# Performance work log

Measured on AMD Instinct MI355X. Metric: run time of the kernel, lower is better.

## Reference

```python
import jax, jax.numpy as jnp
import numpy as np


def setup_inputs() -> dict:
    key = jax.random.key(0)
    ks = jax.random.split(key, 4)
    d, d_k, d_v = 1024, 128, 128
    B, S = 4, 4096
    scale = 1.0 / np.sqrt(d)
    return {
        "X": jax.random.normal(ks[0], (B, S, d), dtype=jnp.float32),
        "W_q": jax.random.normal(ks[1], (d, d_k), dtype=jnp.float32) * scale,
        "b_q": jnp.zeros((d_k,), dtype=jnp.float32),
        "W_k": jax.random.normal(ks[2], (d, d_k), dtype=jnp.float32) * scale,
        "b_k": jnp.zeros((d_k,), dtype=jnp.float32),
        "W_v": jax.random.normal(ks[3], (d, d_v), dtype=jnp.float32) * scale,
        "b_v": jnp.zeros((d_v,), dtype=jnp.float32),
    }


def reference(X, W_q, b_q, W_k, b_k, W_v, b_v):
    # Projections: [B, S, d_k/d_v]
    Q = jnp.einsum("bsd,dk->bsk", X, W_q) + b_q
    K = jnp.einsum("bsd,dk->bsk", X, W_k) + b_k
    V = jnp.einsum("bsd,dv->bsv", X, W_v) + b_v

    d_k = Q.shape[-1]
    # Scaled dot-product scores: [B, S, S]
    scores = jnp.einsum("bqk,bsk->bqs", Q, K) / jnp.sqrt(jnp.float32(d_k))
    # Causal (lower-triangular) mask
    S = scores.shape[-1]
    causal = jnp.tril(jnp.ones((S, S), dtype=bool))
    scores = jnp.where(causal[None, :, :], scores, -jnp.inf)
    weights = jax.nn.softmax(scores, axis=-1)
    # Weighted sum of values: [B, S, d_v]
    return jnp.einsum("bqs,bsv->bqv", weights, V)
```

## Files before the change

### kernel.cpp

```cpp
#include <hip/hip_runtime.h>
#include <hip/hip_bf16.h>
#include <stdint.h>


typedef __bf16 bf16x8 __attribute__((ext_vector_type(8)));
typedef float  f32x4  __attribute__((ext_vector_type(4)));
typedef unsigned int u32x4 __attribute__((ext_vector_type(4)));
typedef unsigned int u32x2 __attribute__((ext_vector_type(2)));

using bf16 = __hip_bfloat16;

#define AS1 __attribute__((address_space(1)))
#define AS3 __attribute__((address_space(3)))

__device__ __forceinline__ void gl_lds16(const void* g, void* l) {
  __builtin_amdgcn_global_load_lds((AS1 uint32_t*)g, (AS3 uint32_t*)l, 16, 0, 0);
}

__device__ __forceinline__ void wait_vm4() {
  asm volatile("s_waitcnt vmcnt(4)" ::: "memory");
  __builtin_amdgcn_sched_barrier(0);
}
__device__ __forceinline__ void wait_vm0() {
  asm volatile("s_waitcnt vmcnt(0)" ::: "memory");
  __builtin_amdgcn_sched_barrier(0);
}

__global__ __launch_bounds__(256) void k_wt(const float* __restrict__ Wq,
                                            const float* __restrict__ Wk,
                                            const float* __restrict__ Wv,
                                            bf16* __restrict__ Wt) {
  __shared__ bf16 t[64][72];
  const float* W = blockIdx.z == 0 ? Wq : (blockIdx.z == 1 ? Wk : Wv);
  int k0 = blockIdx.x * 64, n0 = blockIdx.y * 64;
  int tid = threadIdx.x;
  int r = tid >> 4, c4 = (tid & 15) * 4;
#pragma unroll
  for (int s = 0; s < 4; ++s) {
    int rr = r + s * 16;
    float4 v = *(const float4*)(W + (size_t)(k0 + rr) * 128 + n0 + c4);
    t[rr][c4 + 0] = __float2bfloat16(v.x);
    t[rr][c4 + 1] = __float2bfloat16(v.y);
    t[rr][c4 + 2] = __float2bfloat16(v.z);
    t[rr][c4 + 3] = __float2bfloat16(v.w);
  }
  __syncthreads();
  bf16* out = Wt + (size_t)blockIdx.z * 128 * 1024;
#pragma unroll
  for (int s = 0; s < 4; ++s) {
    int rn = r + s * 16;
    union { bf16 h[4]; u32x2 v; } u;
    u.h[0] = t[c4 + 0][rn]; u.h[1] = t[c4 + 1][rn];
    u.h[2] = t[c4 + 2][rn]; u.h[3] = t[c4 + 3][rn];
    *(u32x2*)(out + (size_t)(n0 + rn) * 1024 + k0 + c4) = u.v;
  }
}

__global__ __launch_bounds__(512) void k_qkv(const float* __restrict__ X,
                                             const bf16* __restrict__ Wt,
                                             const float* __restrict__ bq,
                                             const float* __restrict__ bk,
                                             const float* __restrict__ bv,
                                             bf16* __restrict__ Qo,
                                             bf16* __restrict__ Ko,
                                             bf16* __restrict__ Vt) {
  __shared__ __align__(16) char smem[65536];
  float* Xs = (float*)smem;
  bf16* Ws = (bf16*)(smem + 16384);
  bf16* Vs = (bf16*)smem;

  const int m0 = blockIdx.x * 64;
  const int tid = threadIdx.x;
  const int lane = tid & 63;
  const int li = lane & 15, g = lane >> 4;
  const int wid = tid >> 6;
  const int wm = wid >> 2, wn = wid & 3;

  const int xr = tid >> 3;
  const int xc32 = (tid & 7) >> 1;
  const int xhf = tid & 1;
  const int wr = tid >> 2;
  const int wc = tid & 3;

  f32x4 acc[3][2][2] = {};

  {
    gl_lds16(X + (size_t)(m0 + xr) * 1024 + (xc32 ^ (xr & 3)) * 8 + xhf * 4,
             Xs + tid * 4);
#pragma unroll
    for (int z = 0; z < 3; ++z)
      gl_lds16(Wt + (size_t)z * 131072 + (size_t)wr * 1024 + (wc ^ (wr & 3)) * 8,
               Ws + z * 4096 + tid * 8);
  }
  int cur = 0;
  for (int kt = 0; kt < 32; ++kt) {
    if (kt < 31) {
      const int k0 = (kt + 1) * 32;
      gl_lds16(X + (size_t)(m0 + xr) * 1024 + k0 + (xc32 ^ (xr & 3)) * 8 + xhf * 4,
               Xs + (cur ^ 1) * 2048 + tid * 4);
#pragma unroll
      for (int z = 0; z < 3; ++z)
        gl_lds16(Wt + (size_t)z * 131072 + (size_t)wr * 1024 + k0 + (wc ^ (wr & 3)) * 8,
                 Ws + (cur ^ 1) * 12288 + z * 4096 + tid * 8);
      wait_vm4();
    } else {
      wait_vm0();
    }
    __builtin_amdgcn_s_barrier();

    bf16x8 af[2];
#pragma unroll
    for (int mf = 0; mf < 2; ++mf) {
      int r = wm * 32 + mf * 16 + li;
      const float* xp = Xs + cur * 2048 + r * 32 + ((g ^ (r & 3)) * 8);
      f32x4 x0 = *(const f32x4*)xp;
      f32x4 x1 = *(const f32x4*)(xp + 4);
      union { bf16 h[8]; bf16x8 v; } u;
      u.h[0] = __float2bfloat16(x0[0]); u.h[1] = __float2bfloat16(x0[1]);
      u.h[2] = __float2bfloat16(x0[2]); u.h[3] = __float2bfloat16(x0[3]);
      u.h[4] = __float2bfloat16(x1[0]); u.h[5] = __float2bfloat16(x1[1]);
      u.h[6] = __float2bfloat16(x1[2]); u.h[7] = __float2bfloat16(x1[3]);
      af[mf] = u.v;
    }
#pragma unroll
    for (int z = 0; z < 3; ++z) {
#pragma unroll
      for (int nf = 0; nf < 2; ++nf) {
        int r = wn * 32 + nf * 16 + li;
        bf16x8 bfrag =
            *(const bf16x8*)(Ws + cur * 12288 + z * 4096 + r * 32 + ((g ^ (r & 3)) * 8));
#pragma unroll
        for (int mf = 0; mf < 2; ++mf)
          acc[z][mf][nf] = __builtin_amdgcn_mfma_f32_16x16x32_bf16(
              af[mf], bfrag, acc[z][mf][nf], 0, 0, 0);
      }
    }
    __builtin_amdgcn_s_barrier();
    cur ^= 1;
  }

#pragma unroll
  for (int z = 0; z < 2; ++z) {
    const float* bias = z == 0 ? bq : bk;
    bf16* Out = z == 0 ? Qo : Ko;
    const float scale = z == 0 ? 0.12752404368678202f : 1.0f;
#pragma unroll
    for (int nf = 0; nf < 2; ++nf) {
      int col = wn * 32 + nf * 16 + li;
      float bb = bias[col];
#pragma unroll
      for (int mf = 0; mf < 2; ++mf)
#pragma unroll
        for (int j = 0; j < 4; ++j) {
          int row = m0 + wm * 32 + mf * 16 + g * 4 + j;
          Out[(size_t)row * 128 + col] =
              __float2bfloat16((acc[z][mf][nf][j] + bb) * scale);
        }
    }
  }

  __syncthreads();
#pragma unroll
  for (int nf = 0; nf < 2; ++nf) {
    int col = wn * 32 + nf * 16 + li;
    float bb = bv[col];
#pragma unroll
    for (int mf = 0; mf < 2; ++mf)
#pragma unroll
      for (int j = 0; j < 4; ++j) {
        int row = wm * 32 + mf * 16 + g * 4 + j;
        Vs[row * 136 + col] = __float2bfloat16(acc[2][mf][nf][j] + bb);
      }
  }
  __syncthreads();
  const int b = m0 >> 12;
  const int s_off = m0 & 4095;
#pragma unroll
  for (int t2 = 0; t2 < 2; ++t2) {
    int idx = tid + 512 * t2;
    int dv = idx & 127;
    int sg = idx >> 7;
    union { bf16 h[8]; u32x4 v; } u;
#pragma unroll
    for (int si = 0; si < 8; ++si) u.h[si] = Vs[(sg * 8 + si) * 136 + dv];
    *(u32x4*)(Vt + (size_t)(b * 128 + dv) * 4096 + s_off + sg * 8) = u.v;
  }
}

__global__ __launch_bounds__(512, 4) void k_attn(const bf16* __restrict__ Qb,
                                                 const bf16* __restrict__ Kb,
                                                 const bf16* __restrict__ Vt,
                                                 bf16* __restrict__ o_part,
                                                 float* __restrict__ l_part) {
  __shared__ __align__(16) bf16 Kls[2][64 * 128];
  __shared__ __align__(16) bf16 Vls[2][128 * 64];
  __shared__ __align__(16) bf16 Pls[8][16 * 36];

  const int bid = blockIdx.x;
  const int xcd = bid & 7;
  const int slot = xcd * 72 + (bid >> 3);
  const int b = slot / 144;
  const int s = 143 - (slot - b * 144);
  const int widx = b * 144 + s;
  int qt = 0;
#pragma unroll
  for (int q2 = 1; q2 < 32; ++q2) {
    int M = q2 >> 2;
    if ((M + 1) * (2 * M + (q2 & 3)) <= s) qt = q2;
  }
  const int Mq = qt >> 2;
  const int chunk = s - (Mq + 1) * (2 * Mq + (qt & 3));
  const int ntiles = 2 * qt + 2;
  const int nch = (qt + 4) >> 2;
  const int clen = ntiles / nch;
  const int crem = ntiles - clen * nch;
  const int kt0 = chunk * clen + min(chunk, crem);
  const int kt1 = kt0 + clen + (chunk < crem ? 1 : 0) - 1;

  const int tid = threadIdx.x;
  const int lane = tid & 63;
  const int li = lane & 15, g = lane >> 4;
  const int w8 = tid >> 6;

  bf16x8 qf[4];
#pragma unroll
  for (int ks = 0; ks < 4; ++ks)
    qf[ks] = *(const bf16x8*)(Qb +
        (size_t)(b * 4096 + qt * 128 + w8 * 16 + li) * 128 + ks * 32 + g * 8);

  f32x4 o[8] = {};
  f32x4 lacc = {};
  bf16x8 ones;
#pragma unroll
  for (int e = 0; e < 8; ++e) ones[e] = (__bf16)1.0f;

  bf16* P = &Pls[w8][0];
  const bf16* Vtb = Vt + (size_t)b * 128 * 4096;

  {
    const int kv0 = kt0 * 64;
#pragma unroll
    for (int ii = 0; ii < 2; ++ii) {
      int c = tid + 512 * ii;
      int r = c >> 4, cc = c & 15;
      gl_lds16(Kb + (size_t)(b * 4096 + kv0 + r) * 128 + (cc ^ (r & 7)) * 8,
               &Kls[0][c * 8]);
      int r2 = c >> 3, cc2 = c & 7;
      gl_lds16(Vtb + (size_t)r2 * 4096 + kv0 + (cc2 ^ (r2 & 7)) * 8,
               &Vls[0][c * 8]);
    }
  }
  int cur = 0;
  for (int kt = kt0; kt <= kt1; ++kt) {
    if (kt < kt1) {
      const int kv0n = (kt + 1) * 64;
#pragma unroll
      for (int ii = 0; ii < 2; ++ii) {
        int c = tid + 512 * ii;
        int r = c >> 4, cc = c & 15;
        gl_lds16(Kb + (size_t)(b * 4096 + kv0n + r) * 128 + (cc ^ (r & 7)) * 8,
                 &Kls[cur ^ 1][c * 8]);
        int r2 = c >> 3, cc2 = c & 7;
        gl_lds16(Vtb + (size_t)r2 * 4096 + kv0n + (cc2 ^ (r2 & 7)) * 8,
                 &Vls[cur ^ 1][c * 8]);
      }
      wait_vm4();
    } else {
      wait_vm0();
    }
    __builtin_amdgcn_s_barrier();

    const bf16* Kl = &Kls[cur][0];
    const bf16* Vl = &Vls[cur][0];
    const int kv0 = kt * 64;

    f32x4 st[4] = {};
#pragma unroll
    for (int ks = 0; ks < 4; ++ks) {
      bf16x8 kf[4];
#pragma unroll
      for (int nf = 0; nf < 4; ++nf) {
        int r = nf * 16 + li;
        int ch = (ks * 4 + g) ^ (r & 7);
        kf[nf] = *(const bf16x8*)(Kl + r * 128 + ch * 8);
      }
#pragma unroll
      for (int nf = 0; nf < 4; ++nf)
        st[nf] = __builtin_amdgcn_mfma_f32_16x16x32_bf16(
            kf[nf], qf[ks], st[nf], 0, 0, 0);
    }

    if (kt >= 2 * qt) {
      const int dk = kv0 - qt * 128;
      const int qloc = w8 * 16 + li;
#pragma unroll
      for (int nf = 0; nf < 4; ++nf)
#pragma unroll
        for (int j = 0; j < 4; ++j)
          if (dk + nf * 16 + g * 4 + j > qloc) st[nf][j] = -1e30f;
    }

#pragma unroll
    for (int h = 0; h < 2; ++h) {
#pragma unroll
      for (int nfh = 0; nfh < 2; ++nfh) {
        const f32x4 sv = st[h * 2 + nfh];
        union { bf16 h4[4]; u32x2 v; } u;
#pragma unroll
        for (int j = 0; j < 4; ++j)
          u.h4[j] = __float2bfloat16(exp2f(sv[j]));
        *(u32x2*)(P + li * 36 + nfh * 16 + g * 4) = u.v;
      }
      bf16x8 pa = *(const bf16x8*)(P + li * 36 + g * 8);
#pragma unroll
      for (int dvf = 0; dvf < 8; ++dvf) {
        int r = dvf * 16 + li;
        int ch = (h * 4 + g) ^ (li & 7);
        bf16x8 vf = *(const bf16x8*)(Vl + r * 64 + ch * 8);
        o[dvf] = __builtin_amdgcn_mfma_f32_16x16x32_bf16(
            vf, pa, o[dvf], 0, 0, 0);
      }
      lacc = __builtin_amdgcn_mfma_f32_16x16x32_bf16(ones, pa, lacc, 0, 0, 0);
    }
    __builtin_amdgcn_s_barrier();
    cur ^= 1;
  }

  bf16* op = o_part + (size_t)widx * (128 * 128);
  float* lp = l_part + widx * 128;
  {
    const int qloc = w8 * 16 + li;
    if (g == 0) lp[qloc] = lacc[0];
#pragma unroll
    for (int dvf = 0; dvf < 8; ++dvf) {
      union { bf16 h4[4]; u32x2 v; } u;
#pragma unroll
      for (int j = 0; j < 4; ++j) u.h4[j] = __float2bfloat16(o[dvf][j]);
      *(u32x2*)(op + (size_t)qloc * 128 + dvf * 16 + g * 4) = u.v;
    }
  }
}

__global__ __launch_bounds__(256) void k_comb(const bf16* __restrict__ op,
                                              const float* __restrict__ lp,
                                              float* __restrict__ out) {
  int i = blockIdx.x * 256 + threadIdx.x;
  int row = i >> 4;
  int col8 = (i & 15) * 8;
  int b = row >> 12;
  int rb = row & 4095;
  int qt = rb >> 7;
  int lr = rb & 127;
  int M = qt >> 2;
  int base = b * 144 + (M + 1) * (2 * M + (qt & 3));
  int n = (qt + 4) >> 2;
  float l = 0.0f;
  float acc[8] = {};
  for (int c = 0; c < n; ++c) {
    l += lp[(base + c) * 128 + lr];
    union { bf16 h[8]; u32x4 v; } u;
    u.v = *(const u32x4*)(op + (size_t)(base + c) * 16384 + lr * 128 + col8);
#pragma unroll
    for (int j = 0; j < 8; ++j) acc[j] += __bfloat162float(u.h[j]);
  }
  float linv = 1.0f / l;
  float4 r0, r1;
  r0.x = acc[0] * linv; r0.y = acc[1] * linv;
  r0.z = acc[2] * linv; r0.w = acc[3] * linv;
  r1.x = acc[4] * linv; r1.y = acc[5] * linv;
  r1.z = acc[6] * linv; r1.w = acc[7] * linv;
  ((float4*)out)[i * 2] = r0;
  ((float4*)out)[i * 2 + 1] = r1;
}

extern "C" void kernel_launch(void* const* d_in, const int* in_sizes, int n_in,
                              void* d_out, int out_size, void* d_ws, size_t ws_size,
                              hipStream_t stream) {
  const float* X  = (const float*)d_in[0];
  const float* Wq = (const float*)d_in[1];
  const float* bq = (const float*)d_in[2];
  const float* Wk = (const float*)d_in[3];
  const float* bk = (const float*)d_in[4];
  const float* Wv = (const float*)d_in[5];
  const float* bv = (const float*)d_in[6];
  float* out = (float*)d_out;

  char* ws = (char*)d_ws;
  bf16* Wt  = (bf16*)(ws + 0);
  bf16* Qb  = (bf16*)(ws + 786432);
  bf16* Kb  = (bf16*)(ws + 4980736);
  bf16* Vt  = (bf16*)(ws + 9175040);
  bf16* o_part = (bf16*)(ws + 13369344);
  float* l_part = (float*)(ws + 32243712);

  k_wt<<<dim3(16, 2, 3), dim3(256), 0, stream>>>(Wq, Wk, Wv, Wt);
  k_qkv<<<dim3(256), dim3(512), 0, stream>>>(X, Wt, bq, bk, bv, Qb, Kb, Vt);
  k_attn<<<dim3(576), dim3(512), 0, stream>>>(Qb, Kb, Vt, o_part, l_part);
  k_comb<<<dim3(1024), dim3(256), 0, stream>>>(o_part, l_part, out);
}
```

Measured before the change: 85.05 us.

## Use 32x32x16 MFMA in attention with register-permuted P instead of LDS

The attention kernel now uses 4 waves of 32 query rows each (256 threads) instead of 8 waves of 16, and switches to 32x32x16 bf16 MFMAs for both QK^T and PV. The P matrix is now rearranged into the B-operand layout with ds_bpermute lane exchanges instead of a round trip through a per-wave LDS buffer. The aim is to raise MFMA efficiency, reduce K/V LDS reads per FLOP, and remove the LDS writes and reads of P. In exchange, accumulator register pressure per wave goes up, and there are fewer waves per block to hide load latency.

```diff
diff --git a/kernel.cpp b/kernel.cpp
--- a/kernel.cpp
+++ b/kernel.cpp
@@ -5,6 +5,7 @@
 
 typedef __bf16 bf16x8 __attribute__((ext_vector_type(8)));
 typedef float  f32x4  __attribute__((ext_vector_type(4)));
+typedef float  f32x16 __attribute__((ext_vector_type(16)));
 typedef unsigned int u32x4 __attribute__((ext_vector_type(4)));
 typedef unsigned int u32x2 __attribute__((ext_vector_type(2)));
 
@@ -19,6 +20,10 @@
 
 __device__ __forceinline__ void wait_vm4() {
   asm volatile("s_waitcnt vmcnt(4)" ::: "memory");
+  __builtin_amdgcn_sched_barrier(0);
+}
+__device__ __forceinline__ void wait_vm8() {
+  asm volatile("s_waitcnt vmcnt(8)" ::: "memory");
   __builtin_amdgcn_sched_barrier(0);
 }
 __device__ __forceinline__ void wait_vm0() {
@@ -187,14 +192,13 @@
   }
 }
 
-__global__ __launch_bounds__(512, 4) void k_attn(const bf16* __restrict__ Qb,
+__global__ __launch_bounds__(256, 2) void k_attn(const bf16* __restrict__ Qb,
                                                  const bf16* __restrict__ Kb,
                                                  const bf16* __restrict__ Vt,
                                                  bf16* __restrict__ o_part,
                                                  float* __restrict__ l_part) {
   __shared__ __align__(16) bf16 Kls[2][64 * 128];
   __shared__ __align__(16) bf16 Vls[2][128 * 64];
-  __shared__ __align__(16) bf16 Pls[8][16 * 36];
 
   const int bid = blockIdx.x;
   const int xcd = bid & 7;
@@ -219,29 +223,30 @@
 
   const int tid = threadIdx.x;
   const int lane = tid & 63;
-  const int li = lane & 15, g = lane >> 4;
-  const int w8 = tid >> 6;
-
-  bf16x8 qf[4];
-#pragma unroll
-  for (int ks = 0; ks < 4; ++ks)
-    qf[ks] = *(const bf16x8*)(Qb +
-        (size_t)(b * 4096 + qt * 128 + w8 * 16 + li) * 128 + ks * 32 + g * 8);
-
-  f32x4 o[8] = {};
-  f32x4 lacc = {};
+  const int l31 = lane & 31;
+  const int hl = lane >> 5;
+  const int w = tid >> 6;
+
+  const int qrow = b * 4096 + qt * 128 + w * 32 + l31;
+  bf16x8 qf[8];
+#pragma unroll
+  for (int ks = 0; ks < 8; ++ks)
+    qf[ks] = *(const bf16x8*)(Qb + (size_t)qrow * 128 + ks * 16 + hl * 8);
+
+  f32x16 o[4] = {};
+  f32x16 lacc = {};
   bf16x8 ones;
 #pragma unroll
   for (int e = 0; e < 8; ++e) ones[e] = (__bf16)1.0f;
 
-  bf16* P = &Pls[w8][0];
   const bf16* Vtb = Vt + (size_t)b * 128 * 4096;
+  const int xaddr = (lane ^ 32) << 2;
 
   {
     const int kv0 = kt0 * 64;
 #pragma unroll
-    for (int ii = 0; ii < 2; ++ii) {
-      int c = tid + 512 * ii;
+    for (int ii = 0; ii < 4; ++ii) {
+      int c = tid + 256 * ii;
       int r = c >> 4, cc = c & 15;
       gl_lds16(Kb + (size_t)(b * 4096 + kv0 + r) * 128 + (cc ^ (r & 7)) * 8,
                &Kls[0][c * 8]);
@@ -255,8 +260,8 @@
     if (kt < kt1) {
       const int kv0n = (kt + 1) * 64;
 #pragma unroll
-      for (int ii = 0; ii < 2; ++ii) {
-        int c = tid + 512 * ii;
+      for (int ii = 0; ii < 4; ++ii) {
+        int c = tid + 256 * ii;
         int r = c >> 4, cc = c & 15;
         gl_lds16(Kb + (size_t)(b * 4096 + kv0n + r) * 128 + (cc ^ (r & 7)) * 8,
                  &Kls[cur ^ 1][c * 8]);
@@ -264,7 +269,7 @@
         gl_lds16(Vtb + (size_t)r2 * 4096 + kv0n + (cc2 ^ (r2 & 7)) * 8,
                  &Vls[cur ^ 1][c * 8]);
       }
-      wait_vm4();
+      wait_vm8();
     } else {
       wait_vm0();
     }
@@ -274,53 +279,73 @@
     const bf16* Vl = &Vls[cur][0];
     const int kv0 = kt * 64;
 
-    f32x4 st[4] = {};
-#pragma unroll
-    for (int ks = 0; ks < 4; ++ks) {
-      bf16x8 kf[4];
-#pragma unroll
-      for (int nf = 0; nf < 4; ++nf) {
-        int r = nf * 16 + li;
-        int ch = (ks * 4 + g) ^ (r & 7);
-        kf[nf] = *(const bf16x8*)(Kl + r * 128 + ch * 8);
-      }
-#pragma unroll
-      for (int nf = 0; nf < 4; ++nf)
-        st[nf] = __builtin_amdgcn_mfma_f32_16x16x32_bf16(
-            kf[nf], qf[ks], st[nf], 0, 0, 0);
+    f32x16 st[2] = {};
+#pragma unroll
+    for (int ks = 0; ks < 8; ++ks) {
+#pragma unroll
+      for (int t = 0; t < 2; ++t) {
+        int r = t * 32 + l31;
+        int ch = (2 * ks + hl) ^ (r & 7);
+        bf16x8 kf = *(const bf16x8*)(Kl + r * 128 + ch * 8);
+        st[t] = __builtin_amdgcn_mfma_f32_32x32x16_bf16(
+            kf, qf[ks], st[t], 0, 0, 0);
+      }
     }
 
     if (kt >= 2 * qt) {
       const int dk = kv0 - qt * 128;
-      const int qloc = w8 * 16 + li;
-#pragma unroll
-      for (int nf = 0; nf < 4; ++nf)
-#pragma unroll
-        for (int j = 0; j < 4; ++j)
-          if (dk + nf * 16 + g * 4 + j > qloc) st[nf][j] = -1e30f;
-    }
-
-#pragma unroll
-    for (int h = 0; h < 2; ++h) {
-#pragma unroll
-      for (int nfh = 0; nfh < 2; ++nfh) {
-        const f32x4 sv = st[h * 2 + nfh];
-        union { bf16 h4[4]; u32x2 v; } u;
-#pragma unroll
-        for (int j = 0; j < 4; ++j)
-          u.h4[j] = __float2bfloat16(exp2f(sv[j]));
-        *(u32x2*)(P + li * 36 + nfh * 16 + g * 4) = u.v;
-      }
-      bf16x8 pa = *(const bf16x8*)(P + li * 36 + g * 8);
-#pragma unroll
-      for (int dvf = 0; dvf < 8; ++dvf) {
-        int r = dvf * 16 + li;
-        int ch = (h * 4 + g) ^ (li & 7);
-        bf16x8 vf = *(const bf16x8*)(Vl + r * 64 + ch * 8);
-        o[dvf] = __builtin_amdgcn_mfma_f32_16x16x32_bf16(
-            vf, pa, o[dvf], 0, 0, 0);
-      }
-      lacc = __builtin_amdgcn_mfma_f32_16x16x32_bf16(ones, pa, lacc, 0, 0, 0);
+      const int qloc = w * 32 + l31;
+#pragma unroll
+      for (int t = 0; t < 2; ++t)
+#pragma unroll
+        for (int reg = 0; reg < 16; ++reg) {
+          int kvl = dk + t * 32 + (reg & 3) + 8 * (reg >> 2) + 4 * hl;
+          if (kvl > qloc) st[t][reg] = -1e30f;
+        }
+    }
+
+    uint32_t D[2][8];
+#pragma unroll
+    for (int t = 0; t < 2; ++t)
+#pragma unroll
+      for (int i = 0; i < 8; ++i) {
+        union { bf16 h2[2]; uint32_t u; } pu;
+        pu.h2[0] = __float2bfloat16(exp2f(st[t][2 * i]));
+        pu.h2[1] = __float2bfloat16(exp2f(st[t][2 * i + 1]));
+        D[t][i] = pu.u;
+      }
+
+    uint32_t Z[2][2][2];
+#pragma unroll
+    for (int t = 0; t < 2; ++t)
+#pragma unroll
+      for (int s2 = 0; s2 < 2; ++s2)
+#pragma unroll
+        for (int j = 0; j < 2; ++j) {
+          uint32_t Y = hl ? D[t][4 * s2 + j] : D[t][4 * s2 + 2 + j];
+          Z[t][s2][j] = (uint32_t)__builtin_amdgcn_ds_bpermute(xaddr, (int)Y);
+        }
+
+#pragma unroll
+    for (int t = 0; t < 2; ++t) {
+#pragma unroll
+      for (int s2 = 0; s2 < 2; ++s2) {
+        union { uint32_t u[4]; bf16x8 v; } pb;
+        pb.u[0] = hl ? Z[t][s2][0] : D[t][4 * s2];
+        pb.u[1] = hl ? Z[t][s2][1] : D[t][4 * s2 + 1];
+        pb.u[2] = hl ? D[t][4 * s2 + 2] : Z[t][s2][0];
+        pb.u[3] = hl ? D[t][4 * s2 + 3] : Z[t][s2][1];
+#pragma unroll
+        for (int ds = 0; ds < 4; ++ds) {
+          int r = ds * 32 + l31;
+          int ch = (4 * t + 2 * s2 + hl) ^ (r & 7);
+          bf16x8 vf = *(const bf16x8*)(Vl + r * 64 + ch * 8);
+          o[ds] = __builtin_amdgcn_mfma_f32_32x32x16_bf16(
+              vf, pb.v, o[ds], 0, 0, 0);
+        }
+        lacc = __builtin_amdgcn_mfma_f32_32x32x16_bf16(
+            ones, pb.v, lacc, 0, 0, 0);
+      }
     }
     __builtin_amdgcn_s_barrier();
     cur ^= 1;
@@ -328,17 +353,18 @@
 
   bf16* op = o_part + (size_t)widx * (128 * 128);
   float* lp = l_part + widx * 128;
-  {
-    const int qloc = w8 * 16 + li;
-    if (g == 0) lp[qloc] = lacc[0];
-#pragma unroll
-    for (int dvf = 0; dvf < 8; ++dvf) {
+  const int qloc = w * 32 + l31;
+  if (hl == 0) lp[qloc] = lacc[0];
+#pragma unroll
+  for (int ds = 0; ds < 4; ++ds)
+#pragma unroll
+    for (int a = 0; a < 4; ++a) {
       union { bf16 h4[4]; u32x2 v; } u;
 #pragma unroll
-      for (int j = 0; j < 4; ++j) u.h4[j] = __float2bfloat16(o[dvf][j]);
-      *(u32x2*)(op + (size_t)qloc * 128 + dvf * 16 + g * 4) = u.v;
-    }
-  }
+      for (int j = 0; j < 4; ++j)
+        u.h4[j] = __float2bfloat16(o[ds][4 * a + j]);
+      *(u32x2*)(op + (size_t)qloc * 128 + ds * 32 + 8 * a + 4 * hl) = u.v;
+    }
 }
 
 __global__ __launch_bounds__(256) void k_comb(const bf16* __restrict__ op,
@@ -395,6 +421,6 @@
 
   k_wt<<<dim3(16, 2, 3), dim3(256), 0, stream>>>(Wq, Wk, Wv, Wt);
   k_qkv<<<dim3(256), dim3(512), 0, stream>>>(X, Wt, bq, bk, bv, Qb, Kb, Vt);
-  k_attn<<<dim3(576), dim3(512), 0, stream>>>(Qb, Kb, Vt, o_part, l_part);
+  k_attn<<<dim3(576), dim3(256), 0, stream>>>(Qb, Kb, Vt, o_part, l_part);
   k_comb<<<dim3(1024), dim3(256), 0, stream>>>(o_part, l_part, out);
 }
```

After: 82.13 us. 3.4% less time.
